# Optimization experiments

Measured on AMD Instinct MI355X. Metric: run time of the kernel, lower is better.

Reference implementation:

```python
import jax, jax.numpy as jnp
import numpy as np

THRESHOLD = 0.01
TOPK_RATIO = 0.7

def setup_inputs() -> dict:
    key = jax.random.key(0)
    k1, k2, k3, k4, k5 = jax.random.split(key, 5)
    B, N, F, K = 8, 2048, 512, 256
    x = jax.random.normal(k1, (B, N, F), dtype=jnp.float32)
    adj = jax.random.uniform(k2, (B, N, N), dtype=jnp.float32)
    mask = jnp.ones((B, N), dtype=jnp.float32)
    # assign_main = Linear(F->K), ReLU, Linear(K->K)
    W1 = jax.random.normal(k3, (F, K), dtype=jnp.float32) / np.sqrt(F)
    b1 = jnp.zeros((K,), dtype=jnp.float32)
    W2 = jax.random.normal(k4, (K, K), dtype=jnp.float32) / np.sqrt(K)
    b2 = jnp.zeros((K,), dtype=jnp.float32)
    return {"x": x, "adj": adj, "mask": mask, "W1": W1, "b1": b1, "W2": W2, "b2": b2}

def reference(x, adj, mask, W1, b1, W2, b2):
    B, N, Fdim = x.shape
    K = W2.shape[1]
    # soft assignment logits with masked softmax over clusters
    h = jax.nn.relu(jnp.einsum('bnf,fk->bnk', x, W1) + b1)
    logits = jnp.einsum('bnk,kl->bnl', h, W2) + b2            # [B,N,K]
    logits = logits + (-1e9) * (1.0 - mask[..., None])
    S = jax.nn.softmax(logits, axis=-1)                       # [B,N,K]
    # pooled features and pooled adjacency
    pfeat = jnp.einsum('bnk,bnf->bkf', S, x)                  # S^T x -> [B,K,F]
    mid = jnp.einsum('bnm,bmk->bnk', adj, S)                  # adj @ S
    pooled = jnp.einsum('bnk,bnl->bkl', S, mid)               # S^T adj S -> [B,K,K]
    # threshold + top-k sparsify with straight-through estimator
    topk = min(K, int(np.ceil(TOPK_RATIO * K)))
    thr_mask = (pooled >= THRESHOLD).astype(pooled.dtype)
    a_thr = pooled * thr_mask
    _, idx = jax.lax.top_k(a_thr, topk)                       # [B,K,topk]
    bi = jnp.arange(B)[:, None, None]
    ri = jnp.arange(K)[None, :, None]
    fmask = jnp.zeros_like(pooled).at[bi, ri, idx].set(1.0)
    a_sp = pooled * fmask
    a_ste = a_sp + jax.lax.stop_gradient(pooled - a_sp)       # forward == pooled
    # symmetric degree renormalization
    row_sum = a_ste.sum(axis=-1)
    d_inv_sqrt = 1.0 / jnp.sqrt(row_sum + 1e-9)
    pooled_adj = a_ste * d_inv_sqrt[:, :, None] * d_inv_sqrt[:, None, :]
    pmask = jnp.ones((B, K), dtype=x.dtype)
    return pfeat, pooled_adj, pmask
```

## Files before the change

kernel.cpp:

```cpp
#include <hip/hip_runtime.h>
#include <hip/hip_bf16.h>


typedef float f32x4 __attribute__((ext_vector_type(4)));
typedef __bf16 bf16x8 __attribute__((ext_vector_type(8)));

#define VMCNT(n) asm volatile("s_waitcnt vmcnt(" #n ")" ::: "memory")
#define LGKM0    asm volatile("s_waitcnt lgkmcnt(0)" ::: "memory")
#define SCHEDB   __builtin_amdgcn_sched_barrier(0)
#define BARRIER                                        \
  do {                                                 \
    LGKM0;                                             \
    __builtin_amdgcn_s_barrier();                      \
    asm volatile("" ::: "memory");                     \
    SCHEDB;                                            \
  } while (0)

__device__ __forceinline__ void async_load16(const void* g, void* l) {
  __builtin_amdgcn_global_load_lds((const __attribute__((address_space(1))) void*)g,
                                   (__attribute__((address_space(3))) void*)l, 16, 0, 0);
}
__device__ __forceinline__ unsigned short f2bf(float f) {
  return __builtin_bit_cast(unsigned short, (__bf16)f);
}
__device__ __forceinline__ ushort4 f4_to_bf4(float4 v) {
  ushort4 u; u.x = f2bf(v.x); u.y = f2bf(v.y); u.z = f2bf(v.z); u.w = f2bf(v.w); return u;
}

template <int ROWS, int BK, int NT>
__device__ __forceinline__ void stage_bf16(const __bf16* __restrict__ src, long long ld,
                                           __bf16* lds, int t) {
  constexpr int GR = BK / 8;
  constexpr int N = ROWS * GR / NT;
#pragma unroll
  for (int c = 0; c < N; ++c) {
    const int idx = c * NT + t;
    const int row = idx / GR;
    const int g = idx % GR;
    const int gs = g ^ (row & (GR - 1) & 7);
    async_load16(src + (long long)row * ld + gs * 8, lds + idx * 8);
  }
}
template <int BK>
__device__ __forceinline__ bf16x8 frag(const __bf16* lds, int row, int kq) {
  constexpr int GR = BK / 8;
  const int g = kq ^ (row & (GR - 1) & 7);
  return *(const bf16x8*)(lds + row * BK + g * 8);
}

__global__ __launch_bounds__(256) void prep_weights_k(const float* __restrict__ W1,
                                                      const float* __restrict__ W2,
                                                      __bf16* __restrict__ W1T,
                                                      __bf16* __restrict__ W2T) {
  __shared__ float tile[64][65];
  int bid = blockIdx.x;
  const float* in; __bf16* out; int R, C;
  if (bid < 32) { in = W1; out = W1T; R = 512; C = 256; }
  else { bid -= 32; in = W2; out = W2T; R = 256; C = 256; }
  const int r0 = (bid >> 2) * 64, c0 = (bid & 3) * 64;
  const int tr = threadIdx.x >> 6, tc = threadIdx.x & 63;
#pragma unroll
  for (int i = 0; i < 16; ++i)
    tile[tr + i * 4][tc] = in[(long long)(r0 + tr + i * 4) * C + c0 + tc];
  __syncthreads();
#pragma unroll
  for (int i = 0; i < 16; ++i)
    out[(long long)(c0 + tr + i * 4) * R + r0 + tc] = (__bf16)tile[tc][tr + i * 4];
}

__device__ __forceinline__ void asg_compute(const __bf16* __restrict__ Abuf,
                                            const __bf16* __restrict__ Bbuf,
                                            f32x4 (&acc)[2][4], int wn, int l15, int l4) {
  bf16x8 af[2], bf[4];
#pragma unroll
  for (int i = 0; i < 2; ++i) af[i] = frag<32>(Abuf, i * 16 + l15, l4);
#pragma unroll
  for (int j = 0; j < 4; ++j) bf[j] = frag<32>(Bbuf, wn + j * 16 + l15, l4);
  __builtin_amdgcn_s_setprio(1);
#pragma unroll
  for (int i = 0; i < 2; ++i)
#pragma unroll
    for (int j = 0; j < 4; ++j)
      acc[i][j] = __builtin_amdgcn_mfma_f32_16x16x32_bf16(af[i], bf[j], acc[i][j], 0, 0, 0);
  __builtin_amdgcn_s_setprio(0);
}

__global__ __launch_bounds__(256) void assign_fused_k(
    const float* __restrict__ x, const __bf16* __restrict__ W1T,
    const __bf16* __restrict__ W2T, const float* __restrict__ b1,
    const float* __restrict__ b2, const float* __restrict__ mask,
    __bf16* __restrict__ ST) {
  __shared__ alignas(16) __bf16 Ax[2][32 * 32];
  __shared__ alignas(16) __bf16 Bw[2][256 * 32];
  __shared__ alignas(16) __bf16 hl[32 * 264];
  __shared__ float red[2][4][32];

  const int t = threadIdx.x;
  const int lane = t & 63, wave = t >> 6;
  const int l15 = lane & 15, l4 = lane >> 4;
  const int wn = wave * 64;
  const long long row0 = (long long)blockIdx.x * 32;
  const float* Xb = x + row0 * 512;

  const int arow = t >> 3, afq = t & 7;
  const int ag = afq >> 1;
  const int aoff = arow * 32 + ((ag ^ (arow & 3)) * 8) + (afq & 1) * 4;

  auto ldx = [&](int tile) -> float4 {
    return *(const float4*)(Xb + (long long)arow * 512 + tile * 32 + afq * 4);
  };
  auto sta = [&](__bf16* dst, float4 v) { *(ushort4*)&dst[aoff] = f4_to_bf4(v); };

  f32x4 acc[2][4] = {};

  float4 xA = ldx(0);
  SCHEDB;
  stage_bf16<256, 32, 256>(W1T, 512, Bw[0], t);
  SCHEDB;
  VMCNT(4); SCHEDB;
  sta(Ax[0], xA);
  float4 xB = ldx(1);
  SCHEDB;
  VMCNT(1); SCHEDB;
  BARRIER;

#pragma unroll 1
  for (int tt = 0; tt < 14; tt += 2) {
    stage_bf16<256, 32, 256>(W1T + (tt + 1) * 32, 512, Bw[1], t);
    SCHEDB;
    xA = ldx(tt + 2);
    SCHEDB;
    asg_compute(Ax[0], Bw[0], acc, wn, l15, l4);
    VMCNT(5); SCHEDB;
    sta(Ax[1], xB);
    VMCNT(1); SCHEDB;
    BARRIER;
    stage_bf16<256, 32, 256>(W1T + (tt + 2) * 32, 512, Bw[0], t);
    SCHEDB;
    xB = ldx(tt + 3);
    SCHEDB;
    asg_compute(Ax[1], Bw[1], acc, wn, l15, l4);
    VMCNT(5); SCHEDB;
    sta(Ax[0], xA);
    VMCNT(1); SCHEDB;
    BARRIER;
  }
  stage_bf16<256, 32, 256>(W1T + 15 * 32, 512, Bw[1], t);
  SCHEDB;
  asg_compute(Ax[0], Bw[0], acc, wn, l15, l4);
  VMCNT(4); SCHEDB;
  sta(Ax[1], xB);
  VMCNT(0); SCHEDB;
  BARRIER;
  asg_compute(Ax[1], Bw[1], acc, wn, l15, l4);

  stage_bf16<256, 32, 256>(W2T, 256, Bw[0], t);
  SCHEDB;
#pragma unroll
  for (int j = 0; j < 4; ++j) {
    const int col = wn + j * 16 + l15;
    const float bv = b1[col];
#pragma unroll
    for (int i = 0; i < 2; ++i)
#pragma unroll
      for (int r = 0; r < 4; ++r)
        hl[(i * 16 + l4 * 4 + r) * 264 + col] = (__bf16)fmaxf(acc[i][j][r] + bv, 0.f);
  }
  VMCNT(0); SCHEDB;
  BARRIER;

  f32x4 acc2[2][4] = {};
#pragma unroll 1
  for (int tt = 0; tt < 8; ++tt) {
    if (tt < 7) stage_bf16<256, 32, 256>(W2T + (tt + 1) * 32, 256, Bw[(tt & 1) ^ 1], t);
    SCHEDB;
    const __bf16* Bc = Bw[tt & 1];
    bf16x8 af[2], bf[4];
#pragma unroll
    for (int i = 0; i < 2; ++i)
      af[i] = *(const bf16x8*)(&hl[(i * 16 + l15) * 264 + tt * 32 + l4 * 8]);
#pragma unroll
    for (int j = 0; j < 4; ++j) bf[j] = frag<32>(Bc, wn + j * 16 + l15, l4);
#pragma unroll
    for (int i = 0; i < 2; ++i)
#pragma unroll
      for (int j = 0; j < 4; ++j)
        acc2[i][j] = __builtin_amdgcn_mfma_f32_16x16x32_bf16(af[i], bf[j], acc2[i][j], 0, 0, 0);
    VMCNT(0); SCHEDB;
    BARRIER;
  }

  float mb[2][4], mx[2][4], sm[2][4];
#pragma unroll
  for (int i = 0; i < 2; ++i)
#pragma unroll
    for (int r = 0; r < 4; ++r) {
      mb[i][r] = -1e9f * (1.0f - mask[row0 + i * 16 + l4 * 4 + r]);
      mx[i][r] = -3.4e38f;
      sm[i][r] = 0.f;
    }
#pragma unroll
  for (int j = 0; j < 4; ++j) {
    const float bv = b2[wn + j * 16 + l15];
#pragma unroll
    for (int i = 0; i < 2; ++i)
#pragma unroll
      for (int r = 0; r < 4; ++r) {
        const float v = acc2[i][j][r] + bv + mb[i][r];
        acc2[i][j][r] = v;
        mx[i][r] = fmaxf(mx[i][r], v);
      }
  }
#pragma unroll
  for (int i = 0; i < 2; ++i)
#pragma unroll
    for (int r = 0; r < 4; ++r) {
      float m = mx[i][r];
      m = fmaxf(m, __shfl_xor(m, 1, 64)); m = fmaxf(m, __shfl_xor(m, 2, 64));
      m = fmaxf(m, __shfl_xor(m, 4, 64)); m = fmaxf(m, __shfl_xor(m, 8, 64));
      mx[i][r] = m;
    }
  if (l15 == 0)
#pragma unroll
    for (int i = 0; i < 2; ++i)
#pragma unroll
      for (int r = 0; r < 4; ++r) red[0][wave][i * 16 + l4 * 4 + r] = mx[i][r];
  __syncthreads();
#pragma unroll
  for (int i = 0; i < 2; ++i)
#pragma unroll
    for (int r = 0; r < 4; ++r) {
      const int rl = i * 16 + l4 * 4 + r;
      mx[i][r] = fmaxf(fmaxf(red[0][0][rl], red[0][1][rl]),
                       fmaxf(red[0][2][rl], red[0][3][rl]));
    }
#pragma unroll
  for (int j = 0; j < 4; ++j)
#pragma unroll
    for (int i = 0; i < 2; ++i)
#pragma unroll
      for (int r = 0; r < 4; ++r) {
        const float e = __expf(acc2[i][j][r] - mx[i][r]);
        acc2[i][j][r] = e;
        sm[i][r] += e;
      }
#pragma unroll
  for (int i = 0; i < 2; ++i)
#pragma unroll
    for (int r = 0; r < 4; ++r) {
      float s = sm[i][r];
      s += __shfl_xor(s, 1, 64); s += __shfl_xor(s, 2, 64);
      s += __shfl_xor(s, 4, 64); s += __shfl_xor(s, 8, 64);
      sm[i][r] = s;
    }
  if (l15 == 0)
#pragma unroll
    for (int i = 0; i < 2; ++i)
#pragma unroll
      for (int r = 0; r < 4; ++r) red[1][wave][i * 16 + l4 * 4 + r] = sm[i][r];
  __syncthreads();
  float inv[2][4];
#pragma unroll
  for (int i = 0; i < 2; ++i)
#pragma unroll
    for (int r = 0; r < 4; ++r) {
      const int rl = i * 16 + l4 * 4 + r;
      inv[i][r] = 1.0f / (red[1][0][rl] + red[1][1][rl] + red[1][2][rl] + red[1][3][rl]);
    }
  const long long bb = row0 >> 11;
  const long long n0 = row0 & 2047;
  __bf16* Sb = ST + bb * 524288;
#pragma unroll
  for (int j = 0; j < 4; ++j) {
    const int col = wn + j * 16 + l15;
#pragma unroll
    for (int i = 0; i < 2; ++i) {
      ushort4 u;
      u.x = f2bf(acc2[i][j][0] * inv[i][0]);
      u.y = f2bf(acc2[i][j][1] * inv[i][1]);
      u.z = f2bf(acc2[i][j][2] * inv[i][2]);
      u.w = f2bf(acc2[i][j][3] * inv[i][3]);
      *(ushort4*)(Sb + (long long)col * 2048 + n0 + i * 16 + l4 * 4) = u;
    }
  }
}

__device__ __forceinline__ void adj_compute(const __bf16* __restrict__ Abuf,
                                            const __bf16* __restrict__ Bbuf,
                                            f32x4 (&acc)[2][4],
                                            int wm, int wn, int l15, int l4) {
#pragma unroll
  for (int ks = 0; ks < 2; ++ks) {
    bf16x8 af[2], bf[4];
#pragma unroll
    for (int i = 0; i < 2; ++i) af[i] = frag<64>(Abuf, wm + i * 16 + l15, ks * 4 + l4);
#pragma unroll
    for (int j = 0; j < 4; ++j) bf[j] = frag<64>(Bbuf, wn + j * 16 + l15, ks * 4 + l4);
    __builtin_amdgcn_s_setprio(1);
#pragma unroll
    for (int i = 0; i < 2; ++i)
#pragma unroll
      for (int j = 0; j < 4; ++j)
        acc[i][j] = __builtin_amdgcn_mfma_f32_16x16x32_bf16(af[i], bf[j], acc[i][j], 0, 0, 0);
    __builtin_amdgcn_s_setprio(0);
  }
}

__global__ __launch_bounds__(512) void gemm_adj_k(const float* __restrict__ adj,
                                                  const __bf16* __restrict__ ST,
                                                  __bf16* __restrict__ midT) {
  __shared__ alignas(16) __bf16 Aa[2][64 * 64];
  __shared__ alignas(16) __bf16 Bs[2][256 * 64];
  const int t = threadIdx.x;
  const int lane = t & 63, wave = t >> 6;
  const int l15 = lane & 15, l4 = lane >> 4;
  const int wm = (wave >> 2) * 32, wn = (wave & 3) * 64;
  const int id = blockIdx.x;
  const int bz = id & 7;
  const long long r0 = (long long)(id >> 3) * 64;
  const float* Ab = adj + (long long)bz * 4194304 + r0 * 2048;
  const __bf16* Bb = ST + (long long)bz * 524288;

  const int arow = t >> 4, afq = t & 15;
  const int ag = afq >> 1;
  const int aoff0 = arow * 64 + ((ag ^ (arow & 7)) * 8) + (afq & 1) * 4;
  const int aoff1 = (arow + 32) * 64 + ((ag ^ ((arow + 32) & 7)) * 8) + (afq & 1) * 4;

  auto lda4 = [&](int tile, int half) -> float4 {
    return *(const float4*)(Ab + (long long)(arow + half * 32) * 2048 + tile * 64 + afq * 4);
  };
  auto sta = [&](__bf16* dst, float4 v0, float4 v1) {
    *(ushort4*)&dst[aoff0] = f4_to_bf4(v0);
    *(ushort4*)&dst[aoff1] = f4_to_bf4(v1);
  };

  f32x4 acc[2][4] = {};

  float4 aA0 = lda4(0, 0), aA1 = lda4(0, 1);
  SCHEDB;
  stage_bf16<256, 64, 512>(Bb, 2048, Bs[0], t);
  SCHEDB;
  VMCNT(4); SCHEDB;
  sta(Aa[0], aA0, aA1);
  float4 aB0 = lda4(1, 0), aB1 = lda4(1, 1);
  SCHEDB;
  VMCNT(2); SCHEDB;
  BARRIER;

#pragma unroll 1
  for (int tt = 0; tt < 30; tt += 2) {
    stage_bf16<256, 64, 512>(Bb + (tt + 1) * 64, 2048, Bs[1], t);
    SCHEDB;
    aA0 = lda4(tt + 2, 0); aA1 = lda4(tt + 2, 1);
    SCHEDB;
    adj_compute(Aa[0], Bs[0], acc, wm, wn, l15, l4);
    VMCNT(6); SCHEDB;
    sta(Aa[1], aB0, aB1);
    VMCNT(2); SCHEDB;
    BARRIER;
    stage_bf16<256, 64, 512>(Bb + (tt + 2) * 64, 2048, Bs[0], t);
    SCHEDB;
    aB0 = lda4(tt + 3, 0); aB1 = lda4(tt + 3, 1);
    SCHEDB;
    adj_compute(Aa[1], Bs[1], acc, wm, wn, l15, l4);
    VMCNT(6); SCHEDB;
    sta(Aa[0], aA0, aA1);
    VMCNT(2); SCHEDB;
    BARRIER;
  }
  stage_bf16<256, 64, 512>(Bb + 31 * 64, 2048, Bs[1], t);
  SCHEDB;
  adj_compute(Aa[0], Bs[0], acc, wm, wn, l15, l4);
  VMCNT(4); SCHEDB;
  sta(Aa[1], aB0, aB1);
  VMCNT(0); SCHEDB;
  BARRIER;
  adj_compute(Aa[1], Bs[1], acc, wm, wn, l15, l4);

  __bf16* Cb = midT + (long long)bz * 524288;
#pragma unroll
  for (int j = 0; j < 4; ++j) {
    const int l = wn + j * 16 + l15;
#pragma unroll
    for (int i = 0; i < 2; ++i) {
      ushort4 u;
      u.x = f2bf(acc[i][j][0]); u.y = f2bf(acc[i][j][1]);
      u.z = f2bf(acc[i][j][2]); u.w = f2bf(acc[i][j][3]);
      *(ushort4*)(Cb + (long long)l * 2048 + r0 + wm + i * 16 + l4 * 4) = u;
    }
  }
}

__device__ __forceinline__ void feat_compute(const __bf16* __restrict__ Abuf,
                                             const __bf16* __restrict__ Bbuf,
                                             f32x4 (&acc)[8][2],
                                             int wm, int wn, int l15, int l4) {
  bf16x8 af[8], bf[2];
#pragma unroll
  for (int i = 0; i < 8; ++i) af[i] = frag<32>(Abuf, wm + i * 16 + l15, l4);
#pragma unroll
  for (int j = 0; j < 2; ++j)
    bf[j] = *(const bf16x8*)(&Bbuf[(wn + j * 16 + l15) * 40 + l4 * 8]);
  __builtin_amdgcn_s_setprio(1);
#pragma unroll
  for (int i = 0; i < 8; ++i)
#pragma unroll
    for (int j = 0; j < 2; ++j)
      acc[i][j] = __builtin_amdgcn_mfma_f32_16x16x32_bf16(af[i], bf[j], acc[i][j], 0, 0, 0);
  __builtin_amdgcn_s_setprio(0);
}

__global__ __launch_bounds__(512) void gemm_feat_k(const __bf16* __restrict__ ST,
                                                   const float* __restrict__ x,
                                                   float* __restrict__ partF) {
  __shared__ alignas(16) __bf16 As[2][256 * 32];
  __shared__ alignas(16) __bf16 Bx[2][128 * 40];
  const int t = threadIdx.x;
  const int lane = t & 63, wave = t >> 6;
  const int l15 = lane & 15, l4 = lane >> 4;
  const int wm = (wave >> 2) * 128, wn = (wave & 3) * 32;
  const int gid = blockIdx.x;
  const int b = gid & 7, ks = gid >> 5, fblk = (gid >> 3) & 3;
  const int f0 = fblk * 128;
  const __bf16* Ab = ST + (long long)b * 524288 + ks * 256;
  const float* Xb = x + (long long)b * 1048576 + (long long)ks * 256 * 512 + f0;

  const int xn0 = t >> 5, xfq = t & 31;
  f32x4 acc[8][2] = {};

  auto ldx = [&](int tile, int half) -> float4 {
    return *(const float4*)(Xb + (long long)(tile * 32 + half * 16 + xn0) * 512 + xfq * 4);
  };
  auto stx = [&](__bf16* dst, float4 v, int half) {
    const int n = half * 16 + xn0;
    dst[(xfq * 4 + 0) * 40 + n] = (__bf16)v.x;
    dst[(xfq * 4 + 1) * 40 + n] = (__bf16)v.y;
    dst[(xfq * 4 + 2) * 40 + n] = (__bf16)v.z;
    dst[(xfq * 4 + 3) * 40 + n] = (__bf16)v.w;
  };

  float4 xA0 = ldx(0, 0), xA1 = ldx(0, 1);
  SCHEDB;
  stage_bf16<256, 32, 512>(Ab, 2048, As[0], t);
  SCHEDB;
  VMCNT(2); SCHEDB;
  stx(Bx[0], xA0, 0); stx(Bx[0], xA1, 1);
  float4 xB0 = ldx(1, 0), xB1 = ldx(1, 1);
  SCHEDB;
  VMCNT(2); SCHEDB;
  BARRIER;

#pragma unroll 1
  for (int tt = 0; tt < 6; tt += 2) {
    stage_bf16<256, 32, 512>(Ab + (tt + 1) * 32, 2048, As[1], t);
    SCHEDB;
    xA0 = ldx(tt + 2, 0); xA1 = ldx(tt + 2, 1);
    SCHEDB;
    feat_compute(As[0], Bx[0], acc, wm, wn, l15, l4);
    VMCNT(4); SCHEDB;
    stx(Bx[1], xB0, 0); stx(Bx[1], xB1, 1);
    VMCNT(2); SCHEDB;
    BARRIER;
    stage_bf16<256, 32, 512>(Ab + (tt + 2) * 32, 2048, As[0], t);
    SCHEDB;
    xB0 = ldx(tt + 3, 0); xB1 = ldx(tt + 3, 1);
    SCHEDB;
    feat_compute(As[1], Bx[1], acc, wm, wn, l15, l4);
    VMCNT(4); SCHEDB;
    stx(Bx[0], xA0, 0); stx(Bx[0], xA1, 1);
    VMCNT(2); SCHEDB;
    BARRIER;
  }
  stage_bf16<256, 32, 512>(Ab + 7 * 32, 2048, As[1], t);
  SCHEDB;
  feat_compute(As[0], Bx[0], acc, wm, wn, l15, l4);
  VMCNT(2); SCHEDB;
  stx(Bx[1], xB0, 0); stx(Bx[1], xB1, 1);
  VMCNT(0); SCHEDB;
  BARRIER;
  feat_compute(As[1], Bx[1], acc, wm, wn, l15, l4);

  float* out = partF + ((long long)b * 8 + ks) * 131072;
#pragma unroll
  for (int i = 0; i < 8; ++i)
#pragma unroll
    for (int j = 0; j < 2; ++j)
#pragma unroll
      for (int r = 0; r < 4; ++r)
        out[(wm + i * 16 + l4 * 4 + r) * 512 + f0 + wn + j * 16 + l15] = acc[i][j][r];
}

__global__ __launch_bounds__(256) void gemm_pool_k(const __bf16* __restrict__ ST,
                                                   const __bf16* __restrict__ midT,
                                                   float* __restrict__ partP) {
  __shared__ alignas(16) __bf16 As[2][64 * 64];
  __shared__ alignas(16) __bf16 Bs[2][64 * 64];
  const int t = threadIdx.x;
  const int lane = t & 63, wave = t >> 6;
  const int l15 = lane & 15, l4 = lane >> 4;
  const int wm = (wave >> 1) * 32, wn = (wave & 1) * 32;
  const int b = blockIdx.z >> 2, ks = blockIdx.z & 3;
  const long long row0 = (long long)blockIdx.y * 64, col0 = (long long)blockIdx.x * 64;
  const __bf16* Ab = ST + (long long)b * 524288 + row0 * 2048 + ks * 512;
  const __bf16* Bb = midT + (long long)b * 524288 + col0 * 2048 + ks * 512;

  f32x4 acc[2][2] = {};
  stage_bf16<64, 64, 256>(Ab, 2048, As[0], t);
  stage_bf16<64, 64, 256>(Bb, 2048, Bs[0], t);
  __syncthreads();
  for (int tt = 0; tt < 8; ++tt) {
    const int cur = tt & 1, nxt = cur ^ 1;
    if (tt < 7) {
      stage_bf16<64, 64, 256>(Ab + (tt + 1) * 64, 2048, As[nxt], t);
      stage_bf16<64, 64, 256>(Bb + (tt + 1) * 64, 2048, Bs[nxt], t);
    }
#pragma unroll
    for (int ksb = 0; ksb < 2; ++ksb) {
      bf16x8 af[2], bfr[2];
#pragma unroll
      for (int i = 0; i < 2; ++i) af[i] = frag<64>(As[cur], wm + i * 16 + l15, ksb * 4 + l4);
#pragma unroll
      for (int j = 0; j < 2; ++j) bfr[j] = frag<64>(Bs[cur], wn + j * 16 + l15, ksb * 4 + l4);
#pragma unroll
      for (int i = 0; i < 2; ++i)
#pragma unroll
        for (int j = 0; j < 2; ++j)
          acc[i][j] = __builtin_amdgcn_mfma_f32_16x16x32_bf16(af[i], bfr[j], acc[i][j], 0, 0, 0);
    }
    __syncthreads();
  }
  float* out = partP + (long long)blockIdx.z * 65536;
#pragma unroll
  for (int i = 0; i < 2; ++i)
#pragma unroll
    for (int j = 0; j < 2; ++j)
#pragma unroll
      for (int r = 0; r < 4; ++r)
        out[(row0 + wm + i * 16 + l4 * 4 + r) * 256 + col0 + wn + j * 16 + l15] = acc[i][j][r];
}

__global__ __launch_bounds__(256) void reduce_pool_k(const float* __restrict__ partP,
                                                     float* __restrict__ pooled,
                                                     float* __restrict__ dinv) {
  const int gr = blockIdx.x * 4 + (threadIdx.x >> 6);
  const int lane = threadIdx.x & 63;
  const int b = gr >> 8, row = gr & 255;
  const long long base = (long long)b * 4 * 65536 + (long long)row * 256;
  float s = 0.f;
#pragma unroll
  for (int q = 0; q < 4; ++q) {
    const int c = lane + q * 64;
    float v = partP[base + c] + partP[base + 65536 + c] +
              partP[base + 131072 + c] + partP[base + 196608 + c];
    pooled[(long long)gr * 256 + c] = v;
    s += v;
  }
#pragma unroll
  for (int o = 32; o > 0; o >>= 1) s += __shfl_xor(s, o, 64);
  if (lane == 0) dinv[gr] = rsqrtf(s + 1e-9f);
}

__global__ __launch_bounds__(256) void reduce_feat_k(const float* __restrict__ partF,
                                                     float* __restrict__ pfeat) {
  const long long p = blockIdx.x * 256LL + threadIdx.x;
  const int b = (int)(p >> 15), rc = (int)(p & 32767);
  const float4* src = (const float4*)partF;
  float4 a = {0.f, 0.f, 0.f, 0.f};
#pragma unroll
  for (int ks = 0; ks < 8; ++ks) {
    const float4 v = src[(long long)(b * 8 + ks) * 32768 + rc];
    a.x += v.x; a.y += v.y; a.z += v.z; a.w += v.w;
  }
  ((float4*)pfeat)[p] = a;
}

__global__ __launch_bounds__(256) void finalize_k(const float* __restrict__ pooled,
                                                  const float* __restrict__ dinv,
                                                  float* __restrict__ outAdj,
                                                  float* __restrict__ pmask) {
  const long long i = blockIdx.x * 256LL + threadIdx.x;
  const int c = (int)(i & 255);
  const int r = (int)((i >> 8) & 255);
  const int b = (int)(i >> 16);
  outAdj[i] = pooled[i] * dinv[b * 256 + r] * dinv[b * 256 + c];
  if (i < 2048) pmask[i] = 1.0f;
}

extern "C" void kernel_launch(void* const* d_in, const int* in_sizes, int n_in,
                              void* d_out, int out_size, void* d_ws, size_t ws_size,
                              hipStream_t stream) {
  (void)in_sizes; (void)n_in; (void)out_size; (void)ws_size;
  const float* x    = (const float*)d_in[0];
  const float* adj  = (const float*)d_in[1];
  const float* mask = (const float*)d_in[2];
  const float* W1   = (const float*)d_in[3];
  const float* b1   = (const float*)d_in[4];
  const float* W2   = (const float*)d_in[5];
  const float* b2   = (const float*)d_in[6];

  char* ws = (char*)d_ws;
  __bf16* ST     = (__bf16*)(ws + 0);
  __bf16* midT   = (__bf16*)(ws + 8388608);
  float*  partP  = (float*)(ws + 16777216);
  float*  partF  = (float*)(ws + 25165824);
  float*  pooled = (float*)(ws + 58720256);
  float*  dinv   = (float*)(ws + 60817408);
  __bf16* W1T    = (__bf16*)(ws + 60825600);
  __bf16* W2T    = (__bf16*)(ws + 61087744);

  float* pfeat  = (float*)d_out;
  float* outAdj = (float*)d_out + 1048576;
  float* pmask  = (float*)d_out + 1572864;

  prep_weights_k<<<48, 256, 0, stream>>>(W1, W2, W1T, W2T);
  assign_fused_k<<<512, 256, 0, stream>>>(x, W1T, W2T, b1, b2, mask, ST);
  gemm_feat_k<<<256, 512, 0, stream>>>(ST, x, partF);
  reduce_feat_k<<<1024, 256, 0, stream>>>(partF, pfeat);
  gemm_adj_k<<<256, 512, 0, stream>>>(adj, ST, midT);
  gemm_pool_k<<<dim3(4, 4, 32), 256, 0, stream>>>(ST, midT, partP);
  reduce_pool_k<<<512, 256, 0, stream>>>(partP, pooled, dinv);
  finalize_k<<<2048, 256, 0, stream>>>(pooled, dinv, outAdj, pmask);
}
```

Baseline: 116.5 us.

## Drop split-K partials, pretranspose x to bf16, retile GEMMs to 512 blocks

The prep kernel now also transposes x into a bf16 [F,N] buffer, so the feature GEMM becomes a plain bf16 NT GEMM over full K without split-K partials or a reduction kernel. The pool GEMM also drops split-K, writes pooled directly, and replaces reduce_pool with a plain rowsum. The adjacency GEMM moves from 64-row/512-thread blocks to 32-row/256-thread blocks so all three GEMMs launch 512 blocks, with the vmcnt waits adjusted. This removes partial-buffer traffic and two reduction launches. The cost is an extra 16MB read and 8MB write to transpose x, and longer serial K loops with smaller tiles that get less reuse per block.

```diff
diff --git a/kernel.cpp b/kernel.cpp
--- a/kernel.cpp
+++ b/kernel.cpp
@@ -32,6 +32,7 @@
                                            __bf16* lds, int t) {
   constexpr int GR = BK / 8;
   constexpr int N = ROWS * GR / NT;
+  static_assert(N >= 1, "stage too small");
 #pragma unroll
   for (int c = 0; c < N; ++c) {
     const int idx = c * NT + t;
@@ -48,17 +49,28 @@
   return *(const bf16x8*)(lds + row * BK + g * 8);
 }
 
-__global__ __launch_bounds__(256) void prep_weights_k(const float* __restrict__ W1,
-                                                      const float* __restrict__ W2,
-                                                      __bf16* __restrict__ W1T,
-                                                      __bf16* __restrict__ W2T) {
+__global__ __launch_bounds__(256) void prep_k(const float* __restrict__ x,
+                                              const float* __restrict__ W1,
+                                              const float* __restrict__ W2,
+                                              __bf16* __restrict__ xbT,
+                                              __bf16* __restrict__ W1T,
+                                              __bf16* __restrict__ W2T) {
   __shared__ float tile[64][65];
-  int bid = blockIdx.x;
-  const float* in; __bf16* out; int R, C;
-  if (bid < 32) { in = W1; out = W1T; R = 512; C = 256; }
-  else { bid -= 32; in = W2; out = W2T; R = 256; C = 256; }
-  const int r0 = (bid >> 2) * 64, c0 = (bid & 3) * 64;
   const int tr = threadIdx.x >> 6, tc = threadIdx.x & 63;
+  const int bid = blockIdx.x;
+  const float* in; __bf16* out; int r0, c0, C, R;
+  if (bid < 2048) {
+    const int fb = bid >> 8, rest = bid & 255;
+    const int nb = rest >> 3, b = rest & 7;
+    in = x + (long long)b * 1048576; out = xbT + (long long)b * 1048576;
+    r0 = nb * 64; c0 = fb * 64; R = 2048; C = 512;
+  } else if (bid < 2080) {
+    const int w = bid - 2048;
+    in = W1; out = W1T; r0 = (w >> 2) * 64; c0 = (w & 3) * 64; R = 512; C = 256;
+  } else {
+    const int w = bid - 2080;
+    in = W2; out = W2T; r0 = (w >> 2) * 64; c0 = (w & 3) * 64; R = 256; C = 256;
+  }
 #pragma unroll
   for (int i = 0; i < 16; ++i)
     tile[tr + i * 4][tc] = in[(long long)(r0 + tr + i * 4) * C + c0 + tc];
@@ -288,12 +300,12 @@
 __device__ __forceinline__ void adj_compute(const __bf16* __restrict__ Abuf,
                                             const __bf16* __restrict__ Bbuf,
                                             f32x4 (&acc)[2][4],
-                                            int wm, int wn, int l15, int l4) {
+                                            int wn, int l15, int l4) {
 #pragma unroll
   for (int ks = 0; ks < 2; ++ks) {
     bf16x8 af[2], bf[4];
 #pragma unroll
-    for (int i = 0; i < 2; ++i) af[i] = frag<64>(Abuf, wm + i * 16 + l15, ks * 4 + l4);
+    for (int i = 0; i < 2; ++i) af[i] = frag<64>(Abuf, i * 16 + l15, ks * 4 + l4);
 #pragma unroll
     for (int j = 0; j < 4; ++j) bf[j] = frag<64>(Bbuf, wn + j * 16 + l15, ks * 4 + l4);
     __builtin_amdgcn_s_setprio(1);
@@ -306,28 +318,28 @@
   }
 }
 
-__global__ __launch_bounds__(512) void gemm_adj_k(const float* __restrict__ adj,
+__global__ __launch_bounds__(256) void gemm_adj_k(const float* __restrict__ adj,
                                                   const __bf16* __restrict__ ST,
                                                   __bf16* __restrict__ midT) {
-  __shared__ alignas(16) __bf16 Aa[2][64 * 64];
+  __shared__ alignas(16) __bf16 Aa[2][32 * 64];
   __shared__ alignas(16) __bf16 Bs[2][256 * 64];
   const int t = threadIdx.x;
   const int lane = t & 63, wave = t >> 6;
   const int l15 = lane & 15, l4 = lane >> 4;
-  const int wm = (wave >> 2) * 32, wn = (wave & 3) * 64;
+  const int wn = wave * 64;
   const int id = blockIdx.x;
   const int bz = id & 7;
-  const long long r0 = (long long)(id >> 3) * 64;
+  const long long r0 = (long long)(id >> 3) * 32;
   const float* Ab = adj + (long long)bz * 4194304 + r0 * 2048;
   const __bf16* Bb = ST + (long long)bz * 524288;
 
   const int arow = t >> 4, afq = t & 15;
   const int ag = afq >> 1;
   const int aoff0 = arow * 64 + ((ag ^ (arow & 7)) * 8) + (afq & 1) * 4;
-  const int aoff1 = (arow + 32) * 64 + ((ag ^ ((arow + 32) & 7)) * 8) + (afq & 1) * 4;
+  const int aoff1 = (arow + 16) * 64 + ((ag ^ ((arow + 16) & 7)) * 8) + (afq & 1) * 4;
 
   auto lda4 = [&](int tile, int half) -> float4 {
-    return *(const float4*)(Ab + (long long)(arow + half * 32) * 2048 + tile * 64 + afq * 4);
+    return *(const float4*)(Ab + (long long)(arow + half * 16) * 2048 + tile * 64 + afq * 4);
   };
   auto sta = [&](__bf16* dst, float4 v0, float4 v1) {
     *(ushort4*)&dst[aoff0] = f4_to_bf4(v0);
@@ -338,9 +350,9 @@
 
   float4 aA0 = lda4(0, 0), aA1 = lda4(0, 1);
   SCHEDB;
-  stage_bf16<256, 64, 512>(Bb, 2048, Bs[0], t);
-  SCHEDB;
-  VMCNT(4); SCHEDB;
+  stage_bf16<256, 64, 256>(Bb, 2048, Bs[0], t);
+  SCHEDB;
+  VMCNT(8); SCHEDB;
   sta(Aa[0], aA0, aA1);
   float4 aB0 = lda4(1, 0), aB1 = lda4(1, 1);
   SCHEDB;
@@ -349,33 +361,33 @@
 
 #pragma unroll 1
   for (int tt = 0; tt < 30; tt += 2) {
-    stage_bf16<256, 64, 512>(Bb + (tt + 1) * 64, 2048, Bs[1], t);
+    stage_bf16<256, 64, 256>(Bb + (tt + 1) * 64, 2048, Bs[1], t);
     SCHEDB;
     aA0 = lda4(tt + 2, 0); aA1 = lda4(tt + 2, 1);
     SCHEDB;
-    adj_compute(Aa[0], Bs[0], acc, wm, wn, l15, l4);
-    VMCNT(6); SCHEDB;
+    adj_compute(Aa[0], Bs[0], acc, wn, l15, l4);
+    VMCNT(10); SCHEDB;
     sta(Aa[1], aB0, aB1);
     VMCNT(2); SCHEDB;
     BARRIER;
-    stage_bf16<256, 64, 512>(Bb + (tt + 2) * 64, 2048, Bs[0], t);
+    stage_bf16<256, 64, 256>(Bb + (tt + 2) * 64, 2048, Bs[0], t);
     SCHEDB;
     aB0 = lda4(tt + 3, 0); aB1 = lda4(tt + 3, 1);
     SCHEDB;
-    adj_compute(Aa[1], Bs[1], acc, wm, wn, l15, l4);
-    VMCNT(6); SCHEDB;
+    adj_compute(Aa[1], Bs[1], acc, wn, l15, l4);
+    VMCNT(10); SCHEDB;
     sta(Aa[0], aA0, aA1);
     VMCNT(2); SCHEDB;
     BARRIER;
   }
-  stage_bf16<256, 64, 512>(Bb + 31 * 64, 2048, Bs[1], t);
-  SCHEDB;
-  adj_compute(Aa[0], Bs[0], acc, wm, wn, l15, l4);
-  VMCNT(4); SCHEDB;
+  stage_bf16<256, 64, 256>(Bb + 31 * 64, 2048, Bs[1], t);
+  SCHEDB;
+  adj_compute(Aa[0], Bs[0], acc, wn, l15, l4);
+  VMCNT(8); SCHEDB;
   sta(Aa[1], aB0, aB1);
   VMCNT(0); SCHEDB;
   BARRIER;
-  adj_compute(Aa[1], Bs[1], acc, wm, wn, l15, l4);
+  adj_compute(Aa[1], Bs[1], acc, wn, l15, l4);
 
   __bf16* Cb = midT + (long long)bz * 524288;
 #pragma unroll
@@ -386,192 +398,107 @@
       ushort4 u;
       u.x = f2bf(acc[i][j][0]); u.y = f2bf(acc[i][j][1]);
       u.z = f2bf(acc[i][j][2]); u.w = f2bf(acc[i][j][3]);
-      *(ushort4*)(Cb + (long long)l * 2048 + r0 + wm + i * 16 + l4 * 4) = u;
-    }
-  }
-}
-
-__device__ __forceinline__ void feat_compute(const __bf16* __restrict__ Abuf,
-                                             const __bf16* __restrict__ Bbuf,
-                                             f32x4 (&acc)[8][2],
-                                             int wm, int wn, int l15, int l4) {
-  bf16x8 af[8], bf[2];
-#pragma unroll
-  for (int i = 0; i < 8; ++i) af[i] = frag<32>(Abuf, wm + i * 16 + l15, l4);
-#pragma unroll
-  for (int j = 0; j < 2; ++j)
-    bf[j] = *(const bf16x8*)(&Bbuf[(wn + j * 16 + l15) * 40 + l4 * 8]);
-  __builtin_amdgcn_s_setprio(1);
-#pragma unroll
-  for (int i = 0; i < 8; ++i)
-#pragma unroll
-    for (int j = 0; j < 2; ++j)
-      acc[i][j] = __builtin_amdgcn_mfma_f32_16x16x32_bf16(af[i], bf[j], acc[i][j], 0, 0, 0);
-  __builtin_amdgcn_s_setprio(0);
-}
-
-__global__ __launch_bounds__(512) void gemm_feat_k(const __bf16* __restrict__ ST,
-                                                   const float* __restrict__ x,
-                                                   float* __restrict__ partF) {
-  __shared__ alignas(16) __bf16 As[2][256 * 32];
-  __shared__ alignas(16) __bf16 Bx[2][128 * 40];
-  const int t = threadIdx.x;
-  const int lane = t & 63, wave = t >> 6;
-  const int l15 = lane & 15, l4 = lane >> 4;
-  const int wm = (wave >> 2) * 128, wn = (wave & 3) * 32;
-  const int gid = blockIdx.x;
-  const int b = gid & 7, ks = gid >> 5, fblk = (gid >> 3) & 3;
-  const int f0 = fblk * 128;
-  const __bf16* Ab = ST + (long long)b * 524288 + ks * 256;
-  const float* Xb = x + (long long)b * 1048576 + (long long)ks * 256 * 512 + f0;
-
-  const int xn0 = t >> 5, xfq = t & 31;
-  f32x4 acc[8][2] = {};
-
-  auto ldx = [&](int tile, int half) -> float4 {
-    return *(const float4*)(Xb + (long long)(tile * 32 + half * 16 + xn0) * 512 + xfq * 4);
-  };
-  auto stx = [&](__bf16* dst, float4 v, int half) {
-    const int n = half * 16 + xn0;
-    dst[(xfq * 4 + 0) * 40 + n] = (__bf16)v.x;
-    dst[(xfq * 4 + 1) * 40 + n] = (__bf16)v.y;
-    dst[(xfq * 4 + 2) * 40 + n] = (__bf16)v.z;
-    dst[(xfq * 4 + 3) * 40 + n] = (__bf16)v.w;
-  };
-
-  float4 xA0 = ldx(0, 0), xA1 = ldx(0, 1);
-  SCHEDB;
-  stage_bf16<256, 32, 512>(Ab, 2048, As[0], t);
-  SCHEDB;
-  VMCNT(2); SCHEDB;
-  stx(Bx[0], xA0, 0); stx(Bx[0], xA1, 1);
-  float4 xB0 = ldx(1, 0), xB1 = ldx(1, 1);
-  SCHEDB;
-  VMCNT(2); SCHEDB;
-  BARRIER;
-
-#pragma unroll 1
-  for (int tt = 0; tt < 6; tt += 2) {
-    stage_bf16<256, 32, 512>(Ab + (tt + 1) * 32, 2048, As[1], t);
-    SCHEDB;
-    xA0 = ldx(tt + 2, 0); xA1 = ldx(tt + 2, 1);
-    SCHEDB;
-    feat_compute(As[0], Bx[0], acc, wm, wn, l15, l4);
-    VMCNT(4); SCHEDB;
-    stx(Bx[1], xB0, 0); stx(Bx[1], xB1, 1);
-    VMCNT(2); SCHEDB;
-    BARRIER;
-    stage_bf16<256, 32, 512>(Ab + (tt + 2) * 32, 2048, As[0], t);
-    SCHEDB;
-    xB0 = ldx(tt + 3, 0); xB1 = ldx(tt + 3, 1);
-    SCHEDB;
-    feat_compute(As[1], Bx[1], acc, wm, wn, l15, l4);
-    VMCNT(4); SCHEDB;
-    stx(Bx[0], xA0, 0); stx(Bx[0], xA1, 1);
-    VMCNT(2); SCHEDB;
-    BARRIER;
-  }
-  stage_bf16<256, 32, 512>(Ab + 7 * 32, 2048, As[1], t);
-  SCHEDB;
-  feat_compute(As[0], Bx[0], acc, wm, wn, l15, l4);
-  VMCNT(2); SCHEDB;
-  stx(Bx[1], xB0, 0); stx(Bx[1], xB1, 1);
-  VMCNT(0); SCHEDB;
-  BARRIER;
-  feat_compute(As[1], Bx[1], acc, wm, wn, l15, l4);
-
-  float* out = partF + ((long long)b * 8 + ks) * 131072;
-#pragma unroll
-  for (int i = 0; i < 8; ++i)
-#pragma unroll
-    for (int j = 0; j < 2; ++j)
-#pragma unroll
-      for (int r = 0; r < 4; ++r)
-        out[(wm + i * 16 + l4 * 4 + r) * 512 + f0 + wn + j * 16 + l15] = acc[i][j][r];
-}
-
-__global__ __launch_bounds__(256) void gemm_pool_k(const __bf16* __restrict__ ST,
-                                                   const __bf16* __restrict__ midT,
-                                                   float* __restrict__ partP) {
-  __shared__ alignas(16) __bf16 As[2][64 * 64];
+      *(ushort4*)(Cb + (long long)l * 2048 + r0 + i * 16 + l4 * 4) = u;
+    }
+  }
+}
+
+__global__ __launch_bounds__(256) void gemm_feat_k(const __bf16* __restrict__ ST,
+                                                   const __bf16* __restrict__ xbT,
+                                                   float* __restrict__ pfeat) {
+  __shared__ alignas(16) __bf16 As[2][32 * 64];
   __shared__ alignas(16) __bf16 Bs[2][64 * 64];
   const int t = threadIdx.x;
   const int lane = t & 63, wave = t >> 6;
   const int l15 = lane & 15, l4 = lane >> 4;
-  const int wm = (wave >> 1) * 32, wn = (wave & 1) * 32;
-  const int b = blockIdx.z >> 2, ks = blockIdx.z & 3;
-  const long long row0 = (long long)blockIdx.y * 64, col0 = (long long)blockIdx.x * 64;
-  const __bf16* Ab = ST + (long long)b * 524288 + row0 * 2048 + ks * 512;
-  const __bf16* Bb = midT + (long long)b * 524288 + col0 * 2048 + ks * 512;
-
-  f32x4 acc[2][2] = {};
-  stage_bf16<64, 64, 256>(Ab, 2048, As[0], t);
+  const int wn = wave * 16;
+  const int id = blockIdx.x;
+  const int b = id & 7, j7 = id >> 3;
+  const int kblk = j7 & 7, fblk = j7 >> 3;
+  const __bf16* Ab = ST + (long long)b * 524288 + (long long)kblk * 32 * 2048;
+  const __bf16* Bb = xbT + (long long)b * 1048576 + (long long)fblk * 64 * 2048;
+
+  f32x4 acc[2] = {};
+  stage_bf16<32, 64, 256>(Ab, 2048, As[0], t);
   stage_bf16<64, 64, 256>(Bb, 2048, Bs[0], t);
   __syncthreads();
-  for (int tt = 0; tt < 8; ++tt) {
-    const int cur = tt & 1, nxt = cur ^ 1;
-    if (tt < 7) {
-      stage_bf16<64, 64, 256>(Ab + (tt + 1) * 64, 2048, As[nxt], t);
-      stage_bf16<64, 64, 256>(Bb + (tt + 1) * 64, 2048, Bs[nxt], t);
-    }
-#pragma unroll
-    for (int ksb = 0; ksb < 2; ++ksb) {
-      bf16x8 af[2], bfr[2];
-#pragma unroll
-      for (int i = 0; i < 2; ++i) af[i] = frag<64>(As[cur], wm + i * 16 + l15, ksb * 4 + l4);
-#pragma unroll
-      for (int j = 0; j < 2; ++j) bfr[j] = frag<64>(Bs[cur], wn + j * 16 + l15, ksb * 4 + l4);
+#pragma unroll 1
+  for (int tt = 0; tt < 32; ++tt) {
+    const int cur = tt & 1;
+    if (tt < 31) {
+      stage_bf16<32, 64, 256>(Ab + (tt + 1) * 64, 2048, As[cur ^ 1], t);
+      stage_bf16<64, 64, 256>(Bb + (tt + 1) * 64, 2048, Bs[cur ^ 1], t);
+    }
+#pragma unroll
+    for (int ks = 0; ks < 2; ++ks) {
+      bf16x8 af[2], bf;
+#pragma unroll
+      for (int i = 0; i < 2; ++i) af[i] = frag<64>(As[cur], i * 16 + l15, ks * 4 + l4);
+      bf = frag<64>(Bs[cur], wn + l15, ks * 4 + l4);
 #pragma unroll
       for (int i = 0; i < 2; ++i)
-#pragma unroll
-        for (int j = 0; j < 2; ++j)
-          acc[i][j] = __builtin_amdgcn_mfma_f32_16x16x32_bf16(af[i], bfr[j], acc[i][j], 0, 0, 0);
+        acc[i] = __builtin_amdgcn_mfma_f32_16x16x32_bf16(af[i], bf, acc[i], 0, 0, 0);
     }
     __syncthreads();
   }
-  float* out = partP + (long long)blockIdx.z * 65536;
-#pragma unroll
-  for (int i = 0; i < 2; ++i)
-#pragma unroll
-    for (int j = 0; j < 2; ++j)
-#pragma unroll
-      for (int r = 0; r < 4; ++r)
-        out[(row0 + wm + i * 16 + l4 * 4 + r) * 256 + col0 + wn + j * 16 + l15] = acc[i][j][r];
-}
-
-__global__ __launch_bounds__(256) void reduce_pool_k(const float* __restrict__ partP,
-                                                     float* __restrict__ pooled,
-                                                     float* __restrict__ dinv) {
+  float* out = pfeat + (long long)b * 131072;
+#pragma unroll
+  for (int i = 0; i < 2; ++i)
+#pragma unroll
+    for (int r = 0; r < 4; ++r)
+      out[(long long)(kblk * 32 + i * 16 + l4 * 4 + r) * 512 + fblk * 64 + wn + l15] =
+          acc[i][r];
+}
+
+__global__ __launch_bounds__(256) void gemm_pool_k(const __bf16* __restrict__ ST,
+                                                   const __bf16* __restrict__ midT,
+                                                   float* __restrict__ pooled) {
+  __shared__ alignas(16) __bf16 As[2][32 * 64];
+  __shared__ alignas(16) __bf16 Bs[2][32 * 64];
+  const int t = threadIdx.x;
+  const int lane = t & 63, wave = t >> 6;
+  const int l15 = lane & 15, l4 = lane >> 4;
+  const int wm = (wave >> 1) * 16, wn = (wave & 1) * 16;
+  const int id = blockIdx.x;
+  const int b = id & 7, j7 = id >> 3;
+  const int kblk = j7 & 7, lblk = j7 >> 3;
+  const __bf16* Ab = ST + (long long)b * 524288 + (long long)kblk * 32 * 2048;
+  const __bf16* Bb = midT + (long long)b * 524288 + (long long)lblk * 32 * 2048;
+
+  f32x4 acc = {};
+  stage_bf16<32, 64, 256>(Ab, 2048, As[0], t);
+  stage_bf16<32, 64, 256>(Bb, 2048, Bs[0], t);
+  __syncthreads();
+#pragma unroll 1
+  for (int tt = 0; tt < 32; ++tt) {
+    const int cur = tt & 1;
+    if (tt < 31) {
+      stage_bf16<32, 64, 256>(Ab + (tt + 1) * 64, 2048, As[cur ^ 1], t);
+      stage_bf16<32, 64, 256>(Bb + (tt + 1) * 64, 2048, Bs[cur ^ 1], t);
+    }
+#pragma unroll
+    for (int ks = 0; ks < 2; ++ks) {
+      bf16x8 af = frag<64>(As[cur], wm + l15, ks * 4 + l4);
+      bf16x8 bf = frag<64>(Bs[cur], wn + l15, ks * 4 + l4);
+      acc = __builtin_amdgcn_mfma_f32_16x16x32_bf16(af, bf, acc, 0, 0, 0);
+    }
+    __syncthreads();
+  }
+  float* out = pooled + (long long)b * 65536;
+#pragma unroll
+  for (int r = 0; r < 4; ++r)
+    out[(long long)(kblk * 32 + wm + l4 * 4 + r) * 256 + lblk * 32 + wn + l15] = acc[r];
+}
+
+__global__ __launch_bounds__(256) void rowsum_k(const float* __restrict__ pooled,
+                                                float* __restrict__ dinv) {
   const int gr = blockIdx.x * 4 + (threadIdx.x >> 6);
   const int lane = threadIdx.x & 63;
-  const int b = gr >> 8, row = gr & 255;
-  const long long base = (long long)b * 4 * 65536 + (long long)row * 256;
-  float s = 0.f;
-#pragma unroll
-  for (int q = 0; q < 4; ++q) {
-    const int c = lane + q * 64;
-    float v = partP[base + c] + partP[base + 65536 + c] +
-              partP[base + 131072 + c] + partP[base + 196608 + c];
-    pooled[(long long)gr * 256 + c] = v;
-    s += v;
-  }
+  const float* p = pooled + (long long)gr * 256;
+  float s = p[lane] + p[lane + 64] + p[lane + 128] + p[lane + 192];
 #pragma unroll
   for (int o = 32; o > 0; o >>= 1) s += __shfl_xor(s, o, 64);
   if (lane == 0) dinv[gr] = rsqrtf(s + 1e-9f);
-}
-
-__global__ __launch_bounds__(256) void reduce_feat_k(const float* __restrict__ partF,
-                                                     float* __restrict__ pfeat) {
-  const long long p = blockIdx.x * 256LL + threadIdx.x;
-  const int b = (int)(p >> 15), rc = (int)(p & 32767);
-  const float4* src = (const float4*)partF;
-  float4 a = {0.f, 0.f, 0.f, 0.f};
-#pragma unroll
-  for (int ks = 0; ks < 8; ++ks) {
-    const float4 v = src[(long long)(b * 8 + ks) * 32768 + rc];
-    a.x += v.x; a.y += v.y; a.z += v.z; a.w += v.w;
-  }
-  ((float4*)pfeat)[p] = a;
 }
 
 __global__ __launch_bounds__(256) void finalize_k(const float* __restrict__ pooled,
@@ -601,23 +528,21 @@
   char* ws = (char*)d_ws;
   __bf16* ST     = (__bf16*)(ws + 0);
   __bf16* midT   = (__bf16*)(ws + 8388608);
-  float*  partP  = (float*)(ws + 16777216);
-  float*  partF  = (float*)(ws + 25165824);
-  float*  pooled = (float*)(ws + 58720256);
-  float*  dinv   = (float*)(ws + 60817408);
-  __bf16* W1T    = (__bf16*)(ws + 60825600);
-  __bf16* W2T    = (__bf16*)(ws + 61087744);
+  __bf16* xbT    = (__bf16*)(ws + 16777216);
+  float*  pooled = (float*)(ws + 33554432);
+  float*  dinv   = (float*)(ws + 35651584);
+  __bf16* W1T    = (__bf16*)(ws + 35659776);
+  __bf16* W2T    = (__bf16*)(ws + 35921920);
 
   float* pfeat  = (float*)d_out;
   float* outAdj = (float*)d_out + 1048576;
   float* pmask  = (float*)d_out + 1572864;
 
-  prep_weights_k<<<48, 256, 0, stream>>>(W1, W2, W1T, W2T);
+  prep_k<<<2096, 256, 0, stream>>>(x, W1, W2, xbT, W1T, W2T);
   assign_fused_k<<<512, 256, 0, stream>>>(x, W1T, W2T, b1, b2, mask, ST);
-  gemm_feat_k<<<256, 512, 0, stream>>>(ST, x, partF);
-  reduce_feat_k<<<1024, 256, 0, stream>>>(partF, pfeat);
-  gemm_adj_k<<<256, 512, 0, stream>>>(adj, ST, midT);
-  gemm_pool_k<<<dim3(4, 4, 32), 256, 0, stream>>>(ST, midT, partP);
-  reduce_pool_k<<<512, 256, 0, stream>>>(partP, pooled, dinv);
+  gemm_feat_k<<<512, 256, 0, stream>>>(ST, xbT, pfeat);
+  gemm_adj_k<<<512, 256, 0, stream>>>(adj, ST, midT);
+  gemm_pool_k<<<512, 256, 0, stream>>>(ST, midT, pooled);
+  rowsum_k<<<512, 256, 0, stream>>>(pooled, dinv);
   finalize_k<<<2048, 256, 0, stream>>>(pooled, dinv, outAdj, pmask);
 }
```

Measured after the change: 113.4 us. -2.7%, faster.
